# Kernel optimization log

Measured on AMD Instinct MI355X. Metric: run time of the kernel, lower is better.

The kernel has to match this reference:

```python
import jax, jax.numpy as jnp
import numpy as np

NUM_HEADS = 16


def trinity_mask(txt_tok, img_tok):
    """Boolean [N, N] mask, True = attend. Faithful to get_mask(..., 'trinity'):
    - image rows attend block-diagonally within 3 equal image chunks
    - text rows attend to all image tokens and causally to text tokens.
    """
    assert img_tok % 3 == 0, "Invalid text token sizes"
    sit = img_tok // 3
    N = txt_tok + img_tok
    i = jnp.arange(N)[:, None]
    j = jnp.arange(N)[None, :]
    img_img = (i < img_tok) & (j < img_tok) & ((i // sit) == (j // sit))
    txt_img = (i >= img_tok) & (j < img_tok)
    txt_txt = (i >= img_tok) & (j >= img_tok) & (i >= j)
    return img_img | txt_img | txt_txt


def setup_inputs() -> dict:
    key = jax.random.key(0)
    ks = jax.random.split(key, 12)
    B, TXT, IMG = 4, 512, 1536
    N = TXT + IMG
    DQ, DKV = 1024, 1024
    s = lambda d: 1.0 / np.sqrt(d).astype(np.float32)
    return {
        "q": jax.random.normal(ks[0], (B, N, DQ), jnp.float32),
        "kv": jax.random.normal(ks[1], (B, N, DKV), jnp.float32),
        "Wq": jax.random.normal(ks[2], (DQ, DQ), jnp.float32) * s(DQ),
        "bq": jnp.zeros((DQ,), jnp.float32),
        "Wk": jax.random.normal(ks[3], (DKV, DQ), jnp.float32) * s(DKV),
        "bk": jnp.zeros((DQ,), jnp.float32),
        "Wv": jax.random.normal(ks[4], (DKV, DQ), jnp.float32) * s(DKV),
        "bv": jnp.zeros((DQ,), jnp.float32),
        "Wo": jax.random.normal(ks[5], (DQ, DQ), jnp.float32) * s(DQ),
        "bo": jnp.zeros((DQ,), jnp.float32),
        "txt_tok_len": TXT,
        "img_tok_len": IMG,
    }


def reference(q, kv, Wq, bq, Wk, bk, Wv, bv, Wo, bo, txt_tok_len, img_tok_len):
    B, N, C = q.shape
    H = NUM_HEADS
    d = C // H
    scale = d ** -0.5
    # projections, split heads: [B, H, N, d]
    qh = (q @ Wq + bq).reshape(B, N, H, d).transpose(0, 2, 1, 3)
    kh = (kv @ Wk + bk).reshape(B, N, H, d).transpose(0, 2, 1, 3)
    vh = (kv @ Wv + bv).reshape(B, N, H, d).transpose(0, 2, 1, 3)
    scores = jnp.einsum("bhqd,bhkd->bhqk", qh, kh) * scale
    mask = trinity_mask(txt_tok_len, img_tok_len)  # [N, N] bool
    scores = jnp.where(mask[None, None], scores, -jnp.inf)
    attn = jax.nn.softmax(scores, axis=-1)
    # dropout in eval mode -> identity
    out = jnp.einsum("bhqk,bhkd->bhqd", attn, vh)
    out = out.transpose(0, 2, 1, 3).reshape(B, N, C)
    return out @ Wo + bo
```

## Files before the change

kernel.cpp:

```cpp
#include <hip/hip_runtime.h>


typedef _Float16 h16;
typedef _Float16 f16x8 __attribute__((ext_vector_type(8)));
typedef __fp16 fp16v2 __attribute__((ext_vector_type(2)));
typedef float f32x4 __attribute__((ext_vector_type(4)));

#define BATCH 4
#define NTOK  2048
#define CDIM  1024
#define NHEAD 16
#define HDIM  64
#define IMGTOK 1536
#define MROWS (BATCH * NTOK)
#define QSCALE 0.18033688011112042f

__device__ __forceinline__ void gload_lds16(const void* g, void* l) {
  __builtin_amdgcn_global_load_lds(
      (const __attribute__((address_space(1))) unsigned int*)g,
      (__attribute__((address_space(3))) unsigned int*)l, 16, 0, 0);
}

__global__ __launch_bounds__(256)
void cvt_f16(const float* __restrict__ s, h16* __restrict__ d) {
  size_t i = ((size_t)blockIdx.x * 256 + threadIdx.x) * 8;
  float4 a = *(const float4*)(s + i);
  float4 b = *(const float4*)(s + i + 4);
  f16x8 o;
  o[0] = (h16)a.x; o[1] = (h16)a.y; o[2] = (h16)a.z; o[3] = (h16)a.w;
  o[4] = (h16)b.x; o[5] = (h16)b.y; o[6] = (h16)b.z; o[7] = (h16)b.w;
  *(f16x8*)(d + i) = o;
}

__global__ __launch_bounds__(256)
void wtrans(const float* __restrict__ W0, const float* __restrict__ W1,
            const float* __restrict__ W2, const float* __restrict__ W3,
            h16* __restrict__ T0, h16* __restrict__ T1,
            h16* __restrict__ T2, h16* __restrict__ T3) {
  const float* W; h16* T;
  switch (blockIdx.z) {
    case 0: W = W0; T = T0; break;
    case 1: W = W1; T = T1; break;
    case 2: W = W2; T = T2; break;
    default: W = W3; T = T3; break;
  }
  __shared__ float t[32][33];
  const int n0 = blockIdx.x * 32, k0 = blockIdx.y * 32;
  const int tx = threadIdx.x, ty = threadIdx.y;
#pragma unroll
  for (int i = 0; i < 4; i++)
    t[ty + 8 * i][tx] = W[(size_t)(k0 + ty + 8 * i) * CDIM + n0 + tx];
  __syncthreads();
#pragma unroll
  for (int i = 0; i < 4; i++)
    T[(size_t)(n0 + ty + 8 * i) * CDIM + k0 + tx] = (h16)t[tx][ty + 8 * i];
}


__global__ __launch_bounds__(256, 3)
void gemm_qkv(const h16* __restrict__ qb, const h16* __restrict__ kvb,
              const h16* __restrict__ wqt, const h16* __restrict__ wkt,
              const h16* __restrict__ wvt,
              const float* __restrict__ bq, const float* __restrict__ bk,
              const float* __restrict__ bv,
              h16* __restrict__ Qh, h16* __restrict__ Kh,
              h16* __restrict__ VTh) {
  __shared__ __attribute__((aligned(16))) h16 smem[3 * 8192];
  const int id = blockIdx.x;
  const int gid = (id & 7) * 192 + (id >> 3);
  const int which = gid >> 9;
  const int lid = gid & 511;
  const int m0 = (lid >> 3) * 128;
  const int n0 = (lid & 7) * 128;
  const h16* X  = (which == 0) ? qb : kvb;
  const h16* WT = (which == 0) ? wqt : ((which == 1) ? wkt : wvt);
  const float* bias = (which == 0) ? bq : ((which == 1) ? bk : bv);

  const int tid = threadIdx.x;
  const int lane = tid & 63;
  const int w = tid >> 6;
  const int wr = w >> 1, wc = w & 1;
  const int l15 = lane & 15, lhi = lane >> 4;

  f32x4 acc[4][4] = {};

  const int sr = tid >> 2;
  const int pc = tid & 3;
  const int lc = pc ^ ((sr >> 1) & 3);
  const h16* gA0 = X + (size_t)(m0 + sr) * CDIM + lc * 8;
  const h16* gA1 = gA0 + (size_t)64 * CDIM;
  const h16* gB0 = WT + (size_t)(n0 + sr) * CDIM + lc * 8;
  const h16* gB1 = gB0 + (size_t)64 * CDIM;

#define GSTAGE(bi, kt)                                      \
  do {                                                      \
    h16* A_ = smem + (bi) * 8192;                           \
    h16* B_ = A_ + 4096;                                    \
    gload_lds16(gA0 + (kt) * 32, A_ + tid * 8);             \
    gload_lds16(gA1 + (kt) * 32, A_ + (256 + tid) * 8);     \
    gload_lds16(gB0 + (kt) * 32, B_ + tid * 8);             \
    gload_lds16(gB1 + (kt) * 32, B_ + (256 + tid) * 8);     \
  } while (0)

  const int NT = CDIM / 32;
  GSTAGE(0, 0);
  GSTAGE(1, 1);
  const int rswz = (l15 >> 1) & 3;

  int rb = 0, sb = 2;
  for (int kt = 0; kt < NT; ++kt) {
    if (kt + 1 < NT) asm volatile("s_waitcnt vmcnt(4)" ::: "memory");
    else             asm volatile("s_waitcnt vmcnt(0)" ::: "memory");
    __builtin_amdgcn_s_barrier();
    if (kt + 2 < NT) { GSTAGE(sb, kt + 2); sb = (sb == 2) ? 0 : sb + 1; }
    const h16* A_ = smem + rb * 8192;
    const h16* B_ = A_ + 4096;
    rb = (rb == 2) ? 0 : rb + 1;
    f16x8 a[4], bb[4];
#pragma unroll
    for (int i = 0; i < 4; i++)
      a[i] = *(const f16x8*)(A_ + (wr * 64 + i * 16 + l15) * 32 + (lhi ^ rswz) * 8);
#pragma unroll
    for (int i = 0; i < 4; i++)
      bb[i] = *(const f16x8*)(B_ + (wc * 64 + i * 16 + l15) * 32 + (lhi ^ rswz) * 8);
    __builtin_amdgcn_s_setprio(1);
#pragma unroll
    for (int i = 0; i < 4; i++)
#pragma unroll
      for (int j = 0; j < 4; j++)
        acc[i][j] = __builtin_amdgcn_mfma_f32_16x16x32_f16(a[i], bb[j], acc[i][j], 0, 0, 0);
    __builtin_amdgcn_s_setprio(0);
  }
#undef GSTAGE

  if (which == 2) {
    __builtin_amdgcn_s_barrier();
    h16* T = smem;
#pragma unroll
    for (int j = 0; j < 4; j++) {
      const int gcL = wc * 64 + j * 16 + l15;
      const float bval = bias[n0 + gcL];
#pragma unroll
      for (int i = 0; i < 4; i++) {
#pragma unroll
        for (int r = 0; r < 4; r++) {
          const int grL = wr * 64 + i * 16 + lhi * 4 + r;
          const int ch = (grL >> 3) ^ (gcL & 15);
          T[gcL * 128 + ch * 8 + (grL & 7)] = (h16)(acc[i][j][r] + bval);
        }
      }
    }
    __builtin_amdgcn_s_barrier();
    const int bsel = m0 >> 11;
    const int nbase = m0 & (NTOK - 1);
#pragma unroll
    for (int pass = 0; pass < 8; ++pass) {
      const int rowL = pass * 16 + (tid >> 4);
      const int c = tid & 15;
      const int gc = n0 + rowL;
      const int hh = gc >> 6, dd = gc & 63;
      f16x8 v = *(const f16x8*)(T + rowL * 128 + ((c ^ (rowL & 15)) * 8));
      *(f16x8*)(VTh + (((size_t)(bsel * NHEAD + hh)) * HDIM + dd) * NTOK +
                nbase + c * 8) = v;
    }
    return;
  }

  h16* outp = (which == 0) ? Qh : Kh;
  const float scale = (which == 0) ? QSCALE : 1.0f;
#pragma unroll
  for (int j = 0; j < 4; j++) {
    const int gc = n0 + wc * 64 + j * 16 + l15;
    const float bval = bias[gc];
#pragma unroll
    for (int i = 0; i < 4; i++) {
      const int grb = m0 + wr * 64 + i * 16 + lhi * 4;
#pragma unroll
      for (int r = 0; r < 4; r++) {
        const float v = (acc[i][j][r] + bval) * scale;
        const int gr = grb + r;
        const int bidx = gr >> 11, n = gr & (NTOK - 1);
        const int hh = gc >> 6, dd = gc & 63;
        outp[(((size_t)(bidx * NHEAD + hh)) * NTOK + n) * HDIM + dd] = (h16)v;
      }
    }
  }
}

__global__ __launch_bounds__(256, 3)
void gemm_out(const h16* __restrict__ X, const h16* __restrict__ WT,
              const float* __restrict__ bias, float* __restrict__ outp) {
  __shared__ __attribute__((aligned(16))) h16 smem[3 * 8192];
  const int id = blockIdx.x;
  const int gid = (id & 7) * 64 + (id >> 3);
  const int m0 = (gid >> 3) * 128;
  const int n0 = (gid & 7) * 128;

  const int tid = threadIdx.x;
  const int lane = tid & 63;
  const int w = tid >> 6;
  const int wr = w >> 1, wc = w & 1;
  const int l15 = lane & 15, lhi = lane >> 4;

  f32x4 acc[4][4] = {};

  const int sr = tid >> 2;
  const int pc = tid & 3;
  const int lc = pc ^ ((sr >> 1) & 3);
  const h16* gA0 = X + (size_t)(m0 + sr) * CDIM + lc * 8;
  const h16* gA1 = gA0 + (size_t)64 * CDIM;
  const h16* gB0 = WT + (size_t)(n0 + sr) * CDIM + lc * 8;
  const h16* gB1 = gB0 + (size_t)64 * CDIM;

#define GSTAGE(bi, kt)                                      \
  do {                                                      \
    h16* A_ = smem + (bi) * 8192;                           \
    h16* B_ = A_ + 4096;                                    \
    gload_lds16(gA0 + (kt) * 32, A_ + tid * 8);             \
    gload_lds16(gA1 + (kt) * 32, A_ + (256 + tid) * 8);     \
    gload_lds16(gB0 + (kt) * 32, B_ + tid * 8);             \
    gload_lds16(gB1 + (kt) * 32, B_ + (256 + tid) * 8);     \
  } while (0)

  const int NT = CDIM / 32;
  GSTAGE(0, 0);
  GSTAGE(1, 1);
  const int rswz = (l15 >> 1) & 3;

  int rb = 0, sb = 2;
  for (int kt = 0; kt < NT; ++kt) {
    if (kt + 1 < NT) asm volatile("s_waitcnt vmcnt(4)" ::: "memory");
    else             asm volatile("s_waitcnt vmcnt(0)" ::: "memory");
    __builtin_amdgcn_s_barrier();
    if (kt + 2 < NT) { GSTAGE(sb, kt + 2); sb = (sb == 2) ? 0 : sb + 1; }
    const h16* A_ = smem + rb * 8192;
    const h16* B_ = A_ + 4096;
    rb = (rb == 2) ? 0 : rb + 1;
    f16x8 a[4], bb[4];
#pragma unroll
    for (int i = 0; i < 4; i++)
      a[i] = *(const f16x8*)(A_ + (wr * 64 + i * 16 + l15) * 32 + (lhi ^ rswz) * 8);
#pragma unroll
    for (int i = 0; i < 4; i++)
      bb[i] = *(const f16x8*)(B_ + (wc * 64 + i * 16 + l15) * 32 + (lhi ^ rswz) * 8);
    __builtin_amdgcn_s_setprio(1);
#pragma unroll
    for (int i = 0; i < 4; i++)
#pragma unroll
      for (int j = 0; j < 4; j++)
        acc[i][j] = __builtin_amdgcn_mfma_f32_16x16x32_f16(a[i], bb[j], acc[i][j], 0, 0, 0);
    __builtin_amdgcn_s_setprio(0);
  }
#undef GSTAGE

#pragma unroll
  for (int j = 0; j < 4; j++) {
    const int gc = n0 + wc * 64 + j * 16 + l15;
    const float bval = bias[gc];
#pragma unroll
    for (int i = 0; i < 4; i++) {
      const int grb = m0 + wr * 64 + i * 16 + lhi * 4;
#pragma unroll
      for (int r = 0; r < 4; r++)
        outp[(size_t)(grb + r) * CDIM + gc] = acc[i][j][r] + bval;
    }
  }
}

__global__ __launch_bounds__(512, 6)
void attn_kernel(const h16* __restrict__ Qh, const h16* __restrict__ Kh,
                 const h16* __restrict__ VTh, h16* __restrict__ AX) {
  __shared__ __attribute__((aligned(16))) h16 Kb[2][64 * 64];
  __shared__ __attribute__((aligned(16))) h16 Vb[2][64 * 64];
  __shared__ __attribute__((aligned(16))) h16 Pl[8][16 * 64];

  const int tid = threadIdx.x;
  const int lane = tid & 63;
  const int w = tid >> 6;
  const int l15 = lane & 15, lhi = lane >> 4;
  const int lhi4 = lhi * 4;

  const int id = blockIdx.x;
  const int pos = id >> 3;
  const int bh = (id & 7) * 8 + (pos >> 4);
  const int qblk = 15 - (pos & 15);
  const int b = bh >> 4, h = bh & 15;
  const int q0 = qblk * 128;

  const h16* qbase = Qh + (size_t)bh * NTOK * HDIM;
  const h16* kbase = Kh + (size_t)bh * NTOK * HDIM;
  const h16* vbase = VTh + (size_t)bh * HDIM * NTOK;

  const int qrow = q0 + w * 16 + l15;
  const f16x8 qf0 = *(const f16x8*)(qbase + (size_t)qrow * HDIM + lhi * 8);
  const f16x8 qf1 = *(const f16x8*)(qbase + (size_t)qrow * HDIM + 32 + lhi * 8);
  const int qg = qrow;

  const bool is_img = (q0 < IMGTOK);
  const int kstart = is_img ? (q0 & ~511) : 0;
  const int kend = is_img ? (kstart + 512) : (q0 + 128);
  const int nt = (kend - kstart) >> 6;

  float m = -3.0e38f, lp = 0.f;
  f32x4 o[4] = {};

  const int srow = tid >> 3;
  const int scc = (tid & 7) ^ (srow & 7);
#define ASTAGE(bufi, k0s)                                                     \
  do {                                                                        \
    gload_lds16(kbase + (size_t)((k0s) + srow) * HDIM + scc * 8,              \
                Kb[bufi] + tid * 8);                                          \
    gload_lds16(vbase + (size_t)srow * NTOK + (k0s) + scc * 8,                \
                Vb[bufi] + tid * 8);                                          \
  } while (0)

  h16* pl = &Pl[w][0];
  const int x0 = (lhi ^ (l15 & 7)) * 8;
  const int x1 = ((lhi + 4) ^ (l15 & 7)) * 8;
  const int pswz = l15 & 7;
  const int phalf = (lhi & 1) * 4;
  const int plhi2 = lhi >> 1;
  h16* prb = pl + l15 * 64;

  ASTAGE(0, kstart);
  asm volatile("s_waitcnt vmcnt(0)" ::: "memory");
  __builtin_amdgcn_s_barrier();
  int cur = 0;

  for (int t = 0; t < nt; ++t) {
    const int k0 = kstart + t * 64;
    if (t + 1 < nt) ASTAGE(cur ^ 1, k0 + 64);

    const h16* Kc = Kb[cur];
    f32x4 s[4];
    __builtin_amdgcn_s_setprio(1);
#pragma unroll
    for (int hk = 0; hk < 4; ++hk) {
      const h16* kr = Kc + (hk * 16 + l15) * 64;
      const f16x8 kfa = *(const f16x8*)(kr + x0);
      const f16x8 kfb = *(const f16x8*)(kr + x1);
      f32x4 acc = {};
      acc = __builtin_amdgcn_mfma_f32_16x16x32_f16(kfa, qf0, acc, 0, 0, 0);
      acc = __builtin_amdgcn_mfma_f32_16x16x32_f16(kfb, qf1, acc, 0, 0, 0);
      s[hk] = acc;
    }
    __builtin_amdgcn_s_setprio(0);

    const h16* Vc = Vb[cur];
    const h16* vr0 = Vc + l15 * 64;
    const h16* vr1 = Vc + (16 + l15) * 64;
    const f16x8 va0 = *(const f16x8*)(vr0 + x0);
    const f16x8 vb0 = *(const f16x8*)(vr0 + x1);
    const f16x8 va1 = *(const f16x8*)(vr1 + x0);
    const f16x8 vb1 = *(const f16x8*)(vr1 + x1);

    const bool need_mask = (!is_img) && (k0 + 63 >= IMGTOK);
    if (need_mask) {
#pragma unroll
      for (int hk = 0; hk < 4; ++hk)
#pragma unroll
        for (int r = 0; r < 4; ++r) {
          const int kg = k0 + hk * 16 + lhi4 + r;
          if (kg >= IMGTOK && kg > qg) s[hk][r] = -1e30f;
        }
    }
    float lmax = -3.0e38f;
#pragma unroll
    for (int hk = 0; hk < 4; ++hk)
#pragma unroll
      for (int r = 0; r < 4; ++r) lmax = fmaxf(lmax, s[hk][r]);

    if (__any(lmax > m + 8.0f)) {
      float vmax = fmaxf(lmax, __shfl_xor(lmax, 16));
      vmax = fmaxf(vmax, __shfl_xor(vmax, 32));
      const float mnew = fmaxf(m, vmax);
      const float corr = exp2f(m - mnew);
      m = mnew;
      lp *= corr;
      const float c0 = __shfl(corr, lhi4 + 0);
      const float c1 = __shfl(corr, lhi4 + 1);
      const float c2 = __shfl(corr, lhi4 + 2);
      const float c3 = __shfl(corr, lhi4 + 3);
#pragma unroll
      for (int dt = 0; dt < 4; dt++) {
        o[dt][0] *= c0; o[dt][1] *= c1; o[dt][2] *= c2; o[dt][3] *= c3;
      }
    }
#pragma unroll
    for (int hk = 0; hk < 4; ++hk) {
      const float e0 = exp2f(s[hk][0] - m);
      const float e1 = exp2f(s[hk][1] - m);
      const float e2 = exp2f(s[hk][2] - m);
      const float e3 = exp2f(s[hk][3] - m);
      lp += (e0 + e1) + (e2 + e3);
      const fp16v2 lo2 = __builtin_amdgcn_cvt_pkrtz(e0, e1);
      const fp16v2 hi2 = __builtin_amdgcn_cvt_pkrtz(e2, e3);
      uint2 qw;
      qw.x = __builtin_bit_cast(unsigned int, lo2);
      qw.y = __builtin_bit_cast(unsigned int, hi2);
      *(uint2*)(prb + ((hk * 2 + plhi2) ^ pswz) * 8 + phalf) = qw;
    }

    const h16* vr2 = Vc + (32 + l15) * 64;
    const h16* vr3 = Vc + (48 + l15) * 64;
    const f16x8 va2 = *(const f16x8*)(vr2 + x0);
    const f16x8 vb2 = *(const f16x8*)(vr2 + x1);
    const f16x8 va3 = *(const f16x8*)(vr3 + x0);
    const f16x8 vb3 = *(const f16x8*)(vr3 + x1);
    const f16x8 pf0 = *(const f16x8*)(pl + l15 * 64 + x0);
    const f16x8 pf1 = *(const f16x8*)(pl + l15 * 64 + x1);
    asm volatile("s_waitcnt lgkmcnt(0)" ::: "memory");
    __builtin_amdgcn_sched_barrier(0);

    __builtin_amdgcn_s_setprio(1);
    o[0] = __builtin_amdgcn_mfma_f32_16x16x32_f16(pf0, va0, o[0], 0, 0, 0);
    o[0] = __builtin_amdgcn_mfma_f32_16x16x32_f16(pf1, vb0, o[0], 0, 0, 0);
    o[1] = __builtin_amdgcn_mfma_f32_16x16x32_f16(pf0, va1, o[1], 0, 0, 0);
    o[1] = __builtin_amdgcn_mfma_f32_16x16x32_f16(pf1, vb1, o[1], 0, 0, 0);
    o[2] = __builtin_amdgcn_mfma_f32_16x16x32_f16(pf0, va2, o[2], 0, 0, 0);
    o[2] = __builtin_amdgcn_mfma_f32_16x16x32_f16(pf1, vb2, o[2], 0, 0, 0);
    o[3] = __builtin_amdgcn_mfma_f32_16x16x32_f16(pf0, va3, o[3], 0, 0, 0);
    o[3] = __builtin_amdgcn_mfma_f32_16x16x32_f16(pf1, vb3, o[3], 0, 0, 0);
    __builtin_amdgcn_s_setprio(0);

    asm volatile("s_waitcnt vmcnt(0)" ::: "memory");
    __builtin_amdgcn_s_barrier();
    cur ^= 1;
  }
#undef ASTAGE

  float l = lp;
  l += __shfl_xor(l, 16);
  l += __shfl_xor(l, 32);
  const int qg0 = q0 + w * 16 + lhi4;
#pragma unroll
  for (int r = 0; r < 4; r++) {
    const float lr = __shfl(l, lhi4 + r);
    const float inv = 1.0f / lr;
    const size_t row = (size_t)(b * NTOK + qg0 + r);
#pragma unroll
    for (int dt = 0; dt < 4; dt++) {
      const int col = h * 64 + dt * 16 + l15;
      AX[row * CDIM + col] = (h16)(o[dt][r] * inv);
    }
  }
}

extern "C" void kernel_launch(void* const* d_in, const int* in_sizes, int n_in,
                              void* d_out, int out_size, void* d_ws, size_t ws_size,
                              hipStream_t stream) {
  (void)in_sizes; (void)n_in; (void)out_size; (void)ws_size;
  const float* q  = (const float*)d_in[0];
  const float* kv = (const float*)d_in[1];
  const float* Wq = (const float*)d_in[2];
  const float* bq = (const float*)d_in[3];
  const float* Wk = (const float*)d_in[4];
  const float* bk = (const float*)d_in[5];
  const float* Wv = (const float*)d_in[6];
  const float* bv = (const float*)d_in[7];
  const float* Wo = (const float*)d_in[8];
  const float* bo = (const float*)d_in[9];
  float* out = (float*)d_out;

  char* ws = (char*)d_ws;
  const size_t SZ_MK = (size_t)MROWS * CDIM * sizeof(h16);
  const size_t SZ_W  = (size_t)CDIM * CDIM * sizeof(h16);
  h16* qb  = (h16*)(ws);
  h16* kvb = (h16*)(ws + SZ_MK);
  h16* wqt = (h16*)(ws + 2 * SZ_MK);
  h16* wkt = (h16*)(ws + 2 * SZ_MK + SZ_W);
  h16* wvt = (h16*)(ws + 2 * SZ_MK + 2 * SZ_W);
  h16* wot = (h16*)(ws + 2 * SZ_MK + 3 * SZ_W);
  h16* Qh  = (h16*)(ws + 2 * SZ_MK + 4 * SZ_W);
  h16* Kh  = (h16*)(ws + 3 * SZ_MK + 4 * SZ_W);
  h16* VTh = (h16*)(ws + 4 * SZ_MK + 4 * SZ_W);
  h16* ax  = (h16*)(ws);

  cvt_f16<<<4096, 256, 0, stream>>>(q, qb);
  cvt_f16<<<4096, 256, 0, stream>>>(kv, kvb);
  wtrans<<<dim3(32, 32, 4), dim3(32, 8), 0, stream>>>(Wq, Wk, Wv, Wo,
                                                      wqt, wkt, wvt, wot);
  gemm_qkv<<<1536, 256, 0, stream>>>(qb, kvb, wqt, wkt, wvt, bq, bk, bv,
                                     Qh, Kh, VTh);
  attn_kernel<<<1024, 512, 0, stream>>>(Qh, Kh, VTh, ax);
  gemm_out<<<512, 256, 0, stream>>>(ax, wot, bo, out);
}
```

Baseline: 372.9 us.

## Enlarge QKV GEMM tiles to 256x256 and shrink attention blocks to 64 rows

The QKV projection GEMM moves from 128x128 tiles with 256 threads to 256x256 tiles with 512 threads. Each wave now holds 8x4 accumulator fragments, and the V transpose epilogue runs in two halves through LDS. The attention kernel switches from 512-thread blocks covering 128 query rows to 256-thread blocks covering 64 rows, which doubles the grid, and each thread issues two K/V loads per stage. The aim is more operand reuse in the GEMM and finer causal load balance in attention. The cost is fewer, heavier GEMM blocks with more register pressure, and less K/V reuse per attention block.

After: 320.8 us. 14.0% less time.

```diff
diff --git a/kernel.cpp b/kernel.cpp
--- a/kernel.cpp
+++ b/kernel.cpp
@@ -56,8 +56,7 @@
     T[(size_t)(n0 + ty + 8 * i) * CDIM + k0 + tx] = (h16)t[tx][ty + 8 * i];
 }
 
-
-__global__ __launch_bounds__(256, 3)
+__global__ __launch_bounds__(512, 1)
 void gemm_qkv(const h16* __restrict__ qb, const h16* __restrict__ kvb,
               const h16* __restrict__ wqt, const h16* __restrict__ wkt,
               const h16* __restrict__ wvt,
@@ -65,16 +64,142 @@
               const float* __restrict__ bv,
               h16* __restrict__ Qh, h16* __restrict__ Kh,
               h16* __restrict__ VTh) {
-  __shared__ __attribute__((aligned(16))) h16 smem[3 * 8192];
+  __shared__ __attribute__((aligned(16))) h16 smem[3 * 16384];
   const int id = blockIdx.x;
-  const int gid = (id & 7) * 192 + (id >> 3);
-  const int which = gid >> 9;
-  const int lid = gid & 511;
-  const int m0 = (lid >> 3) * 128;
-  const int n0 = (lid & 7) * 128;
+  const int gid = (id & 7) * 48 + (id >> 3);
+  const int which = gid >> 7;
+  const int lid = gid & 127;
+  const int m0 = (lid >> 2) * 256;
+  const int n0 = (lid & 3) * 256;
   const h16* X  = (which == 0) ? qb : kvb;
   const h16* WT = (which == 0) ? wqt : ((which == 1) ? wkt : wvt);
   const float* bias = (which == 0) ? bq : ((which == 1) ? bk : bv);
+
+  const int tid = threadIdx.x;
+  const int lane = tid & 63;
+  const int w = tid >> 6;
+  const int wr = w >> 2, wc = w & 3;
+  const int l15 = lane & 15, lhi = lane >> 4;
+  const int lhi4 = lhi * 4;
+
+  f32x4 acc[8][4] = {};
+
+  const int sr = tid >> 2;
+  const int pc = tid & 3;
+  const int lc = pc ^ ((sr >> 1) & 3);
+  const h16* gA0 = X + (size_t)(m0 + sr) * CDIM + lc * 8;
+  const h16* gA1 = gA0 + (size_t)128 * CDIM;
+  const h16* gB0 = WT + (size_t)(n0 + sr) * CDIM + lc * 8;
+  const h16* gB1 = gB0 + (size_t)128 * CDIM;
+
+#define GSTAGE(bi, kt)                                      \
+  do {                                                      \
+    h16* A_ = smem + (bi) * 16384;                          \
+    h16* B_ = A_ + 8192;                                    \
+    gload_lds16(gA0 + (kt) * 32, A_ + tid * 8);             \
+    gload_lds16(gA1 + (kt) * 32, A_ + (512 + tid) * 8);     \
+    gload_lds16(gB0 + (kt) * 32, B_ + tid * 8);             \
+    gload_lds16(gB1 + (kt) * 32, B_ + (512 + tid) * 8);     \
+  } while (0)
+
+  const int NT = CDIM / 32;
+  GSTAGE(0, 0);
+  GSTAGE(1, 1);
+  const int rswz = (l15 >> 1) & 3;
+
+  int rb = 0, sb = 2;
+  for (int kt = 0; kt < NT; ++kt) {
+    if (kt + 1 < NT) asm volatile("s_waitcnt vmcnt(4)" ::: "memory");
+    else             asm volatile("s_waitcnt vmcnt(0)" ::: "memory");
+    __builtin_amdgcn_s_barrier();
+    if (kt + 2 < NT) { GSTAGE(sb, kt + 2); sb = (sb == 2) ? 0 : sb + 1; }
+    const h16* A_ = smem + rb * 16384;
+    const h16* B_ = A_ + 8192;
+    rb = (rb == 2) ? 0 : rb + 1;
+    f16x8 a[8], bb[4];
+#pragma unroll
+    for (int i = 0; i < 8; i++)
+      a[i] = *(const f16x8*)(A_ + (wr * 128 + i * 16 + l15) * 32 + (lhi ^ rswz) * 8);
+#pragma unroll
+    for (int j = 0; j < 4; j++)
+      bb[j] = *(const f16x8*)(B_ + (wc * 64 + j * 16 + l15) * 32 + (lhi ^ rswz) * 8);
+    __builtin_amdgcn_s_setprio(1);
+#pragma unroll
+    for (int i = 0; i < 8; i++)
+#pragma unroll
+      for (int j = 0; j < 4; j++)
+        acc[i][j] = __builtin_amdgcn_mfma_f32_16x16x32_f16(a[i], bb[j], acc[i][j], 0, 0, 0);
+    __builtin_amdgcn_s_setprio(0);
+  }
+#undef GSTAGE
+
+  if (which == 2) {
+    const int bsel = m0 >> 11;
+    const int nbase = m0 & (NTOK - 1);
+    h16* T = smem;
+    for (int hh2 = 0; hh2 < 2; ++hh2) {
+      __builtin_amdgcn_s_barrier();
+      if ((wc >> 1) == hh2) {
+#pragma unroll
+        for (int j = 0; j < 4; j++) {
+          const int gcL = wc * 64 + j * 16 + l15;
+          const int row = gcL & 127;
+          const float bval = bias[n0 + gcL];
+#pragma unroll
+          for (int i = 0; i < 8; i++) {
+#pragma unroll
+            for (int r = 0; r < 4; r++) {
+              const int grL = wr * 128 + i * 16 + lhi4 + r;
+              const int ch = (grL >> 3) ^ (row & 31);
+              T[row * 256 + ch * 8 + (grL & 7)] = (h16)(acc[i][j][r] + bval);
+            }
+          }
+        }
+      }
+      __builtin_amdgcn_s_barrier();
+#pragma unroll
+      for (int pass = 0; pass < 8; ++pass) {
+        const int rowL = pass * 16 + (tid >> 5);
+        const int c = tid & 31;
+        const int gc = n0 + hh2 * 128 + rowL;
+        const int hh = gc >> 6, dd = gc & 63;
+        f16x8 v = *(const f16x8*)(T + rowL * 256 + ((c ^ (rowL & 31)) * 8));
+        *(f16x8*)(VTh + (((size_t)(bsel * NHEAD + hh)) * HDIM + dd) * NTOK +
+                  nbase + c * 8) = v;
+      }
+    }
+    return;
+  }
+
+  h16* outp = (which == 0) ? Qh : Kh;
+  const float scale = (which == 0) ? QSCALE : 1.0f;
+#pragma unroll
+  for (int j = 0; j < 4; j++) {
+    const int gc = n0 + wc * 64 + j * 16 + l15;
+    const float bval = bias[gc];
+    const int hh = gc >> 6, dd = gc & 63;
+#pragma unroll
+    for (int i = 0; i < 8; i++) {
+      const int grb = m0 + wr * 128 + i * 16 + lhi4;
+#pragma unroll
+      for (int r = 0; r < 4; r++) {
+        const float v = (acc[i][j][r] + bval) * scale;
+        const int gr = grb + r;
+        const int bidx = gr >> 11, n = gr & (NTOK - 1);
+        outp[(((size_t)(bidx * NHEAD + hh)) * NTOK + n) * HDIM + dd] = (h16)v;
+      }
+    }
+  }
+}
+
+__global__ __launch_bounds__(256, 3)
+void gemm_out(const h16* __restrict__ X, const h16* __restrict__ WT,
+              const float* __restrict__ bias, float* __restrict__ outp) {
+  __shared__ __attribute__((aligned(16))) h16 smem[3 * 8192];
+  const int id = blockIdx.x;
+  const int gid = (id & 7) * 64 + (id >> 3);
+  const int m0 = (gid >> 3) * 128;
+  const int n0 = (gid & 7) * 128;
 
   const int tid = threadIdx.x;
   const int lane = tid & 63;
@@ -133,133 +258,13 @@
   }
 #undef GSTAGE
 
-  if (which == 2) {
-    __builtin_amdgcn_s_barrier();
-    h16* T = smem;
-#pragma unroll
-    for (int j = 0; j < 4; j++) {
-      const int gcL = wc * 64 + j * 16 + l15;
-      const float bval = bias[n0 + gcL];
-#pragma unroll
-      for (int i = 0; i < 4; i++) {
-#pragma unroll
-        for (int r = 0; r < 4; r++) {
-          const int grL = wr * 64 + i * 16 + lhi * 4 + r;
-          const int ch = (grL >> 3) ^ (gcL & 15);
-          T[gcL * 128 + ch * 8 + (grL & 7)] = (h16)(acc[i][j][r] + bval);
-        }
-      }
-    }
-    __builtin_amdgcn_s_barrier();
-    const int bsel = m0 >> 11;
-    const int nbase = m0 & (NTOK - 1);
-#pragma unroll
-    for (int pass = 0; pass < 8; ++pass) {
-      const int rowL = pass * 16 + (tid >> 4);
-      const int c = tid & 15;
-      const int gc = n0 + rowL;
-      const int hh = gc >> 6, dd = gc & 63;
-      f16x8 v = *(const f16x8*)(T + rowL * 128 + ((c ^ (rowL & 15)) * 8));
-      *(f16x8*)(VTh + (((size_t)(bsel * NHEAD + hh)) * HDIM + dd) * NTOK +
-                nbase + c * 8) = v;
-    }
-    return;
-  }
-
-  h16* outp = (which == 0) ? Qh : Kh;
-  const float scale = (which == 0) ? QSCALE : 1.0f;
 #pragma unroll
   for (int j = 0; j < 4; j++) {
     const int gc = n0 + wc * 64 + j * 16 + l15;
     const float bval = bias[gc];
 #pragma unroll
     for (int i = 0; i < 4; i++) {
-      const int grb = m0 + wr * 64 + i * 16 + lhi * 4;
-#pragma unroll
-      for (int r = 0; r < 4; r++) {
-        const float v = (acc[i][j][r] + bval) * scale;
-        const int gr = grb + r;
-        const int bidx = gr >> 11, n = gr & (NTOK - 1);
-        const int hh = gc >> 6, dd = gc & 63;
-        outp[(((size_t)(bidx * NHEAD + hh)) * NTOK + n) * HDIM + dd] = (h16)v;
-      }
-    }
-  }
-}
-
-__global__ __launch_bounds__(256, 3)
-void gemm_out(const h16* __restrict__ X, const h16* __restrict__ WT,
-              const float* __restrict__ bias, float* __restrict__ outp) {
-  __shared__ __attribute__((aligned(16))) h16 smem[3 * 8192];
-  const int id = blockIdx.x;
-  const int gid = (id & 7) * 64 + (id >> 3);
-  const int m0 = (gid >> 3) * 128;
-  const int n0 = (gid & 7) * 128;
-
-  const int tid = threadIdx.x;
-  const int lane = tid & 63;
-  const int w = tid >> 6;
-  const int wr = w >> 1, wc = w & 1;
-  const int l15 = lane & 15, lhi = lane >> 4;
-
-  f32x4 acc[4][4] = {};
-
-  const int sr = tid >> 2;
-  const int pc = tid & 3;
-  const int lc = pc ^ ((sr >> 1) & 3);
-  const h16* gA0 = X + (size_t)(m0 + sr) * CDIM + lc * 8;
-  const h16* gA1 = gA0 + (size_t)64 * CDIM;
-  const h16* gB0 = WT + (size_t)(n0 + sr) * CDIM + lc * 8;
-  const h16* gB1 = gB0 + (size_t)64 * CDIM;
-
-#define GSTAGE(bi, kt)                                      \
-  do {                                                      \
-    h16* A_ = smem + (bi) * 8192;                           \
-    h16* B_ = A_ + 4096;                                    \
-    gload_lds16(gA0 + (kt) * 32, A_ + tid * 8);             \
-    gload_lds16(gA1 + (kt) * 32, A_ + (256 + tid) * 8);     \
-    gload_lds16(gB0 + (kt) * 32, B_ + tid * 8);             \
-    gload_lds16(gB1 + (kt) * 32, B_ + (256 + tid) * 8);     \
-  } while (0)
-
-  const int NT = CDIM / 32;
-  GSTAGE(0, 0);
-  GSTAGE(1, 1);
-  const int rswz = (l15 >> 1) & 3;
-
-  int rb = 0, sb = 2;
-  for (int kt = 0; kt < NT; ++kt) {
-    if (kt + 1 < NT) asm volatile("s_waitcnt vmcnt(4)" ::: "memory");
-    else             asm volatile("s_waitcnt vmcnt(0)" ::: "memory");
-    __builtin_amdgcn_s_barrier();
-    if (kt + 2 < NT) { GSTAGE(sb, kt + 2); sb = (sb == 2) ? 0 : sb + 1; }
-    const h16* A_ = smem + rb * 8192;
-    const h16* B_ = A_ + 4096;
-    rb = (rb == 2) ? 0 : rb + 1;
-    f16x8 a[4], bb[4];
-#pragma unroll
-    for (int i = 0; i < 4; i++)
-      a[i] = *(const f16x8*)(A_ + (wr * 64 + i * 16 + l15) * 32 + (lhi ^ rswz) * 8);
-#pragma unroll
-    for (int i = 0; i < 4; i++)
-      bb[i] = *(const f16x8*)(B_ + (wc * 64 + i * 16 + l15) * 32 + (lhi ^ rswz) * 8);
-    __builtin_amdgcn_s_setprio(1);
-#pragma unroll
-    for (int i = 0; i < 4; i++)
-#pragma unroll
-      for (int j = 0; j < 4; j++)
-        acc[i][j] = __builtin_amdgcn_mfma_f32_16x16x32_f16(a[i], bb[j], acc[i][j], 0, 0, 0);
-    __builtin_amdgcn_s_setprio(0);
-  }
-#undef GSTAGE
-
-#pragma unroll
-  for (int j = 0; j < 4; j++) {
-    const int gc = n0 + wc * 64 + j * 16 + l15;
-    const float bval = bias[gc];
-#pragma unroll
-    for (int i = 0; i < 4; i++) {
-      const int grb = m0 + wr * 64 + i * 16 + lhi * 4;
+      const int grb = m0 + wr * 64 + i * 16 + (lhi << 2);
 #pragma unroll
       for (int r = 0; r < 4; r++)
         outp[(size_t)(grb + r) * CDIM + gc] = acc[i][j][r] + bval;
@@ -267,12 +272,12 @@
   }
 }
 
-__global__ __launch_bounds__(512, 6)
+__global__ __launch_bounds__(256)
 void attn_kernel(const h16* __restrict__ Qh, const h16* __restrict__ Kh,
                  const h16* __restrict__ VTh, h16* __restrict__ AX) {
   __shared__ __attribute__((aligned(16))) h16 Kb[2][64 * 64];
   __shared__ __attribute__((aligned(16))) h16 Vb[2][64 * 64];
-  __shared__ __attribute__((aligned(16))) h16 Pl[8][16 * 64];
+  __shared__ __attribute__((aligned(16))) h16 Pl[4][16 * 64];
 
   const int tid = threadIdx.x;
   const int lane = tid & 63;
@@ -282,10 +287,10 @@
 
   const int id = blockIdx.x;
   const int pos = id >> 3;
-  const int bh = (id & 7) * 8 + (pos >> 4);
-  const int qblk = 15 - (pos & 15);
+  const int bh = (id & 7) * 8 + (pos >> 5);
+  const int qblk = 31 - (pos & 31);
   const int b = bh >> 4, h = bh & 15;
-  const int q0 = qblk * 128;
+  const int q0 = qblk * 64;
 
   const h16* qbase = Qh + (size_t)bh * NTOK * HDIM;
   const h16* kbase = Kh + (size_t)bh * NTOK * HDIM;
@@ -297,8 +302,9 @@
   const int qg = qrow;
 
   const bool is_img = (q0 < IMGTOK);
-  const int kstart = is_img ? (q0 & ~511) : 0;
-  const int kend = is_img ? (kstart + 512) : (q0 + 128);
+  int kstart, kend;
+  if (is_img) { kstart = q0 & ~511; kend = kstart + 512; }
+  else        { kstart = 0;         kend = q0 + 64; }
   const int nt = (kend - kstart) >> 6;
 
   float m = -3.0e38f, lp = 0.f;
@@ -310,8 +316,12 @@
   do {                                                                        \
     gload_lds16(kbase + (size_t)((k0s) + srow) * HDIM + scc * 8,              \
                 Kb[bufi] + tid * 8);                                          \
+    gload_lds16(kbase + (size_t)((k0s) + 32 + srow) * HDIM + scc * 8,         \
+                Kb[bufi] + (256 + tid) * 8);                                  \
     gload_lds16(vbase + (size_t)srow * NTOK + (k0s) + scc * 8,                \
                 Vb[bufi] + tid * 8);                                          \
+    gload_lds16(vbase + (size_t)(32 + srow) * NTOK + (k0s) + scc * 8,         \
+                Vb[bufi] + (256 + tid) * 8);                                  \
   } while (0)
 
   h16* pl = &Pl[w][0];
@@ -480,8 +490,8 @@
   cvt_f16<<<4096, 256, 0, stream>>>(kv, kvb);
   wtrans<<<dim3(32, 32, 4), dim3(32, 8), 0, stream>>>(Wq, Wk, Wv, Wo,
                                                       wqt, wkt, wvt, wot);
-  gemm_qkv<<<1536, 256, 0, stream>>>(qb, kvb, wqt, wkt, wvt, bq, bk, bv,
-                                     Qh, Kh, VTh);
-  attn_kernel<<<1024, 512, 0, stream>>>(Qh, Kh, VTh, ax);
+  gemm_qkv<<<384, 512, 0, stream>>>(qb, kvb, wqt, wkt, wvt, bq, bk, bv,
+                                    Qh, Kh, VTh);
+  attn_kernel<<<2048, 256, 0, stream>>>(Qh, Kh, VTh, ax);
   gemm_out<<<512, 256, 0, stream>>>(ax, wot, bo, out);
 }
```

## Widen GEMM K-tile to 64 with double buffering; retile attention to 64-row blocks

Applied to the files above, without the earlier changes.

Both projection GEMMs now share a macro core that stages 64-wide K slices into two LDS buffers instead of three 32-wide buffers. This halves the number of barrier iterations but lowers the occupancy hint to 2 blocks per CU. The attention kernel now uses 256-thread blocks covering 64 query rows, launched as 2048 blocks, with a triple-buffered K/V prefetch running two tiles ahead. The goal is to cut sync overhead and improve load overlap, at the cost of fewer waves per block and more LDS per block.

Result: faster. 311.8 us (-16.4%).

```diff
diff --git a/kernel.cpp b/kernel.cpp
--- a/kernel.cpp
+++ b/kernel.cpp
@@ -57,7 +57,72 @@
 }
 
 
-__global__ __launch_bounds__(256, 3)
+#define GEMM_CORE(X_, WT_)                                                    \
+  f32x4 acc[4][4] = {};                                                       \
+  const int tid = threadIdx.x;                                                \
+  const int lane = tid & 63;                                                  \
+  const int w = tid >> 6;                                                     \
+  const int wr = w >> 1, wc = w & 1;                                          \
+  const int l15 = lane & 15, lhi = lane >> 4;                                 \
+  const int srow = tid >> 3;                    \
+  const int scol = (((tid & 7) ^ (srow & 7)) << 3);    \
+  const h16* gA = X_ + (size_t)(m0 + srow) * CDIM + scol;                     \
+  const h16* gB = WT_ + (size_t)(n0 + srow) * CDIM + scol;                    \
+  const int x0 = ((lhi ^ (l15 & 7)) << 3);                                    \
+  const int x1 = (((lhi + 4) ^ (l15 & 7)) << 3);                              \
+  const int NT = CDIM / 64;                                           \
+  GSTAGE(0, 0);                                                               \
+  for (int kt = 0; kt < NT; ++kt) {                                           \
+    if (kt + 1 < NT) {                                                        \
+      GSTAGE((kt + 1) & 1, kt + 1);                                           \
+      asm volatile("s_waitcnt vmcnt(8)" ::: "memory");                        \
+    } else {                                                                  \
+      asm volatile("s_waitcnt vmcnt(0)" ::: "memory");                        \
+    }                                                                         \
+    __builtin_amdgcn_s_barrier();                                             \
+    const h16* A_ = smem + (kt & 1) * 16384;                                  \
+    const h16* B_ = A_ + 8192;                                                \
+    f16x8 a0[4], a1[4], b0[4], b1[4];                                         \
+    _Pragma("unroll")                                                         \
+    for (int i = 0; i < 4; i++) {                                             \
+      const h16* ar = A_ + (wr * 64 + i * 16 + l15) * 64;                     \
+      a0[i] = *(const f16x8*)(ar + x0);                                       \
+      a1[i] = *(const f16x8*)(ar + x1);                                       \
+    }                                                                         \
+    _Pragma("unroll")                                                         \
+    for (int j = 0; j < 4; j++) {                                             \
+      const h16* br = B_ + (wc * 64 + j * 16 + l15) * 64;                     \
+      b0[j] = *(const f16x8*)(br + x0);                                       \
+      b1[j] = *(const f16x8*)(br + x1);                                       \
+    }                                                                         \
+    __builtin_amdgcn_s_setprio(1);                                            \
+    _Pragma("unroll")                                                         \
+    for (int i = 0; i < 4; i++)                                               \
+      _Pragma("unroll")                                                       \
+      for (int j = 0; j < 4; j++) {                                           \
+        acc[i][j] = __builtin_amdgcn_mfma_f32_16x16x32_f16(a0[i], b0[j],      \
+                                                           acc[i][j], 0, 0, 0);\
+        acc[i][j] = __builtin_amdgcn_mfma_f32_16x16x32_f16(a1[i], b1[j],      \
+                                                           acc[i][j], 0, 0, 0);\
+      }                                                                       \
+    __builtin_amdgcn_s_setprio(0);                                            \
+    __builtin_amdgcn_s_barrier();                                             \
+  }
+
+#define GSTAGE(bi, kt)                                                        \
+  do {                                                                        \
+    h16* A_ = smem + (bi) * 16384;                                            \
+    h16* B_ = A_ + 8192;                                                      \
+    _Pragma("unroll")                                                         \
+    for (int rd = 0; rd < 4; ++rd) {                                          \
+      gload_lds16(gA + (size_t)(rd * 32) * CDIM + (kt) * 64,                  \
+                  A_ + (rd * 256 + tid) * 8);                                 \
+      gload_lds16(gB + (size_t)(rd * 32) * CDIM + (kt) * 64,                  \
+                  B_ + (rd * 256 + tid) * 8);                                 \
+    }                                                                         \
+  } while (0)
+
+__global__ __launch_bounds__(256, 2)
 void gemm_qkv(const h16* __restrict__ qb, const h16* __restrict__ kvb,
               const h16* __restrict__ wqt, const h16* __restrict__ wkt,
               const h16* __restrict__ wvt,
@@ -65,7 +130,7 @@
               const float* __restrict__ bv,
               h16* __restrict__ Qh, h16* __restrict__ Kh,
               h16* __restrict__ VTh) {
-  __shared__ __attribute__((aligned(16))) h16 smem[3 * 8192];
+  __shared__ __attribute__((aligned(16))) h16 smem[2 * 16384];
   const int id = blockIdx.x;
   const int gid = (id & 7) * 192 + (id >> 3);
   const int which = gid >> 9;
@@ -76,63 +141,9 @@
   const h16* WT = (which == 0) ? wqt : ((which == 1) ? wkt : wvt);
   const float* bias = (which == 0) ? bq : ((which == 1) ? bk : bv);
 
-  const int tid = threadIdx.x;
-  const int lane = tid & 63;
-  const int w = tid >> 6;
-  const int wr = w >> 1, wc = w & 1;
-  const int l15 = lane & 15, lhi = lane >> 4;
-
-  f32x4 acc[4][4] = {};
-
-  const int sr = tid >> 2;
-  const int pc = tid & 3;
-  const int lc = pc ^ ((sr >> 1) & 3);
-  const h16* gA0 = X + (size_t)(m0 + sr) * CDIM + lc * 8;
-  const h16* gA1 = gA0 + (size_t)64 * CDIM;
-  const h16* gB0 = WT + (size_t)(n0 + sr) * CDIM + lc * 8;
-  const h16* gB1 = gB0 + (size_t)64 * CDIM;
-
-#define GSTAGE(bi, kt)                                      \
-  do {                                                      \
-    h16* A_ = smem + (bi) * 8192;                           \
-    h16* B_ = A_ + 4096;                                    \
-    gload_lds16(gA0 + (kt) * 32, A_ + tid * 8);             \
-    gload_lds16(gA1 + (kt) * 32, A_ + (256 + tid) * 8);     \
-    gload_lds16(gB0 + (kt) * 32, B_ + tid * 8);             \
-    gload_lds16(gB1 + (kt) * 32, B_ + (256 + tid) * 8);     \
-  } while (0)
-
-  const int NT = CDIM / 32;
-  GSTAGE(0, 0);
-  GSTAGE(1, 1);
-  const int rswz = (l15 >> 1) & 3;
-
-  int rb = 0, sb = 2;
-  for (int kt = 0; kt < NT; ++kt) {
-    if (kt + 1 < NT) asm volatile("s_waitcnt vmcnt(4)" ::: "memory");
-    else             asm volatile("s_waitcnt vmcnt(0)" ::: "memory");
-    __builtin_amdgcn_s_barrier();
-    if (kt + 2 < NT) { GSTAGE(sb, kt + 2); sb = (sb == 2) ? 0 : sb + 1; }
-    const h16* A_ = smem + rb * 8192;
-    const h16* B_ = A_ + 4096;
-    rb = (rb == 2) ? 0 : rb + 1;
-    f16x8 a[4], bb[4];
-#pragma unroll
-    for (int i = 0; i < 4; i++)
-      a[i] = *(const f16x8*)(A_ + (wr * 64 + i * 16 + l15) * 32 + (lhi ^ rswz) * 8);
-#pragma unroll
-    for (int i = 0; i < 4; i++)
-      bb[i] = *(const f16x8*)(B_ + (wc * 64 + i * 16 + l15) * 32 + (lhi ^ rswz) * 8);
-    __builtin_amdgcn_s_setprio(1);
-#pragma unroll
-    for (int i = 0; i < 4; i++)
-#pragma unroll
-      for (int j = 0; j < 4; j++)
-        acc[i][j] = __builtin_amdgcn_mfma_f32_16x16x32_f16(a[i], bb[j], acc[i][j], 0, 0, 0);
-    __builtin_amdgcn_s_setprio(0);
-  }
-#undef GSTAGE
-
+  GEMM_CORE(X, WT)
+
+  const int lhi4 = lhi * 4;
   if (which == 2) {
     __builtin_amdgcn_s_barrier();
     h16* T = smem;
@@ -144,7 +155,7 @@
       for (int i = 0; i < 4; i++) {
 #pragma unroll
         for (int r = 0; r < 4; r++) {
-          const int grL = wr * 64 + i * 16 + lhi * 4 + r;
+          const int grL = wr * 64 + i * 16 + lhi4 + r;
           const int ch = (grL >> 3) ^ (gcL & 15);
           T[gcL * 128 + ch * 8 + (grL & 7)] = (h16)(acc[i][j][r] + bval);
         }
@@ -172,86 +183,31 @@
   for (int j = 0; j < 4; j++) {
     const int gc = n0 + wc * 64 + j * 16 + l15;
     const float bval = bias[gc];
+    const int hh = gc >> 6, dd = gc & 63;
 #pragma unroll
     for (int i = 0; i < 4; i++) {
-      const int grb = m0 + wr * 64 + i * 16 + lhi * 4;
+      const int grb = m0 + wr * 64 + i * 16 + lhi4;
 #pragma unroll
       for (int r = 0; r < 4; r++) {
         const float v = (acc[i][j][r] + bval) * scale;
         const int gr = grb + r;
         const int bidx = gr >> 11, n = gr & (NTOK - 1);
-        const int hh = gc >> 6, dd = gc & 63;
         outp[(((size_t)(bidx * NHEAD + hh)) * NTOK + n) * HDIM + dd] = (h16)v;
       }
     }
   }
 }
 
-__global__ __launch_bounds__(256, 3)
+__global__ __launch_bounds__(256, 2)
 void gemm_out(const h16* __restrict__ X, const h16* __restrict__ WT,
               const float* __restrict__ bias, float* __restrict__ outp) {
-  __shared__ __attribute__((aligned(16))) h16 smem[3 * 8192];
+  __shared__ __attribute__((aligned(16))) h16 smem[2 * 16384];
   const int id = blockIdx.x;
   const int gid = (id & 7) * 64 + (id >> 3);
   const int m0 = (gid >> 3) * 128;
   const int n0 = (gid & 7) * 128;
 
-  const int tid = threadIdx.x;
-  const int lane = tid & 63;
-  const int w = tid >> 6;
-  const int wr = w >> 1, wc = w & 1;
-  const int l15 = lane & 15, lhi = lane >> 4;
-
-  f32x4 acc[4][4] = {};
-
-  const int sr = tid >> 2;
-  const int pc = tid & 3;
-  const int lc = pc ^ ((sr >> 1) & 3);
-  const h16* gA0 = X + (size_t)(m0 + sr) * CDIM + lc * 8;
-  const h16* gA1 = gA0 + (size_t)64 * CDIM;
-  const h16* gB0 = WT + (size_t)(n0 + sr) * CDIM + lc * 8;
-  const h16* gB1 = gB0 + (size_t)64 * CDIM;
-
-#define GSTAGE(bi, kt)                                      \
-  do {                                                      \
-    h16* A_ = smem + (bi) * 8192;                           \
-    h16* B_ = A_ + 4096;                                    \
-    gload_lds16(gA0 + (kt) * 32, A_ + tid * 8);             \
-    gload_lds16(gA1 + (kt) * 32, A_ + (256 + tid) * 8);     \
-    gload_lds16(gB0 + (kt) * 32, B_ + tid * 8);             \
-    gload_lds16(gB1 + (kt) * 32, B_ + (256 + tid) * 8);     \
-  } while (0)
-
-  const int NT = CDIM / 32;
-  GSTAGE(0, 0);
-  GSTAGE(1, 1);
-  const int rswz = (l15 >> 1) & 3;
-
-  int rb = 0, sb = 2;
-  for (int kt = 0; kt < NT; ++kt) {
-    if (kt + 1 < NT) asm volatile("s_waitcnt vmcnt(4)" ::: "memory");
-    else             asm volatile("s_waitcnt vmcnt(0)" ::: "memory");
-    __builtin_amdgcn_s_barrier();
-    if (kt + 2 < NT) { GSTAGE(sb, kt + 2); sb = (sb == 2) ? 0 : sb + 1; }
-    const h16* A_ = smem + rb * 8192;
-    const h16* B_ = A_ + 4096;
-    rb = (rb == 2) ? 0 : rb + 1;
-    f16x8 a[4], bb[4];
-#pragma unroll
-    for (int i = 0; i < 4; i++)
-      a[i] = *(const f16x8*)(A_ + (wr * 64 + i * 16 + l15) * 32 + (lhi ^ rswz) * 8);
-#pragma unroll
-    for (int i = 0; i < 4; i++)
-      bb[i] = *(const f16x8*)(B_ + (wc * 64 + i * 16 + l15) * 32 + (lhi ^ rswz) * 8);
-    __builtin_amdgcn_s_setprio(1);
-#pragma unroll
-    for (int i = 0; i < 4; i++)
-#pragma unroll
-      for (int j = 0; j < 4; j++)
-        acc[i][j] = __builtin_amdgcn_mfma_f32_16x16x32_f16(a[i], bb[j], acc[i][j], 0, 0, 0);
-    __builtin_amdgcn_s_setprio(0);
-  }
-#undef GSTAGE
+  GEMM_CORE(X, WT)
 
 #pragma unroll
   for (int j = 0; j < 4; j++) {
@@ -267,12 +223,12 @@
   }
 }
 
-__global__ __launch_bounds__(512, 6)
+__global__ __launch_bounds__(256)
 void attn_kernel(const h16* __restrict__ Qh, const h16* __restrict__ Kh,
                  const h16* __restrict__ VTh, h16* __restrict__ AX) {
-  __shared__ __attribute__((aligned(16))) h16 Kb[2][64 * 64];
-  __shared__ __attribute__((aligned(16))) h16 Vb[2][64 * 64];
-  __shared__ __attribute__((aligned(16))) h16 Pl[8][16 * 64];
+  __shared__ __attribute__((aligned(16))) h16 Kb[3][64 * 64];
+  __shared__ __attribute__((aligned(16))) h16 Vb[3][64 * 64];
+  __shared__ __attribute__((aligned(16))) h16 Pl[4][16 * 64];
 
   const int tid = threadIdx.x;
   const int lane = tid & 63;
@@ -282,10 +238,10 @@
 
   const int id = blockIdx.x;
   const int pos = id >> 3;
-  const int bh = (id & 7) * 8 + (pos >> 4);
-  const int qblk = 15 - (pos & 15);
+  const int bh = (id & 7) * 8 + (pos >> 5);
+  const int qblk = 31 - (pos & 31);
   const int b = bh >> 4, h = bh & 15;
-  const int q0 = qblk * 128;
+  const int q0 = qblk * 64;
 
   const h16* qbase = Qh + (size_t)bh * NTOK * HDIM;
   const h16* kbase = Kh + (size_t)bh * NTOK * HDIM;
@@ -297,8 +253,9 @@
   const int qg = qrow;
 
   const bool is_img = (q0 < IMGTOK);
-  const int kstart = is_img ? (q0 & ~511) : 0;
-  const int kend = is_img ? (kstart + 512) : (q0 + 128);
+  int kstart, kend;
+  if (is_img) { kstart = q0 & ~511; kend = kstart + 512; }
+  else        { kstart = 0;         kend = q0 + 64; }
   const int nt = (kend - kstart) >> 6;
 
   float m = -3.0e38f, lp = 0.f;
@@ -310,8 +267,12 @@
   do {                                                                        \
     gload_lds16(kbase + (size_t)((k0s) + srow) * HDIM + scc * 8,              \
                 Kb[bufi] + tid * 8);                                          \
+    gload_lds16(kbase + (size_t)((k0s) + 32 + srow) * HDIM + scc * 8,         \
+                Kb[bufi] + (256 + tid) * 8);                                  \
     gload_lds16(vbase + (size_t)srow * NTOK + (k0s) + scc * 8,                \
                 Vb[bufi] + tid * 8);                                          \
+    gload_lds16(vbase + (size_t)(32 + srow) * NTOK + (k0s) + scc * 8,         \
+                Vb[bufi] + (256 + tid) * 8);                                  \
   } while (0)
 
   h16* pl = &Pl[w][0];
@@ -323,13 +284,15 @@
   h16* prb = pl + l15 * 64;
 
   ASTAGE(0, kstart);
-  asm volatile("s_waitcnt vmcnt(0)" ::: "memory");
-  __builtin_amdgcn_s_barrier();
-  int cur = 0;
+  if (nt > 1) ASTAGE(1, kstart + 64);
+  int cur = 0, sb = 2;
 
   for (int t = 0; t < nt; ++t) {
     const int k0 = kstart + t * 64;
-    if (t + 1 < nt) ASTAGE(cur ^ 1, k0 + 64);
+    if (t + 1 < nt) asm volatile("s_waitcnt vmcnt(4)" ::: "memory");
+    else            asm volatile("s_waitcnt vmcnt(0)" ::: "memory");
+    __builtin_amdgcn_s_barrier();
+    if (t + 2 < nt) { ASTAGE(sb, k0 + 128); sb = (sb == 2) ? 0 : sb + 1; }
 
     const h16* Kc = Kb[cur];
     f32x4 s[4];
@@ -423,9 +386,7 @@
     o[3] = __builtin_amdgcn_mfma_f32_16x16x32_f16(pf1, vb3, o[3], 0, 0, 0);
     __builtin_amdgcn_s_setprio(0);
 
-    asm volatile("s_waitcnt vmcnt(0)" ::: "memory");
-    __builtin_amdgcn_s_barrier();
-    cur ^= 1;
+    cur = (cur == 2) ? 0 : cur + 1;
   }
 #undef ASTAGE
 
@@ -482,6 +443,6 @@
                                                       wqt, wkt, wvt, wot);
   gemm_qkv<<<1536, 256, 0, stream>>>(qb, kvb, wqt, wkt, wvt, bq, bk, bv,
                                      Qh, Kh, VTh);
-  attn_kernel<<<1024, 512, 0, stream>>>(Qh, Kh, VTh, ax);
+  attn_kernel<<<2048, 256, 0, stream>>>(Qh, Kh, VTh, ax);
   gemm_out<<<512, 256, 0, stream>>>(ax, wot, bo, out);
 }
```
